# Kernel tuning notes

Measured on AMD Instinct MI355X. Metric: run time of the kernel, lower is better.

## Reference

```python
import jax, jax.numpy as jnp
import numpy as np

N_NODES = 100000
N_EDGES = 1600000
NFEAT, NHID, NCLASS = 512, 128, 40


def setup_inputs() -> dict:
    key = jax.random.key(0)
    ks = jax.random.split(key, 8)
    x = jax.random.normal(ks[0], (N_NODES, NFEAT), dtype=jnp.float32)
    adj_row = jax.random.randint(ks[1], (N_EDGES,), 0, N_NODES, dtype=jnp.int64)
    adj_col = jax.random.randint(ks[2], (N_EDGES,), 0, N_NODES, dtype=jnp.int64)
    adj_val = jax.random.uniform(ks[3], (N_EDGES,), dtype=jnp.float32)
    W1 = jax.random.normal(ks[4], (NFEAT, NHID), dtype=jnp.float32) * (1.0 / np.sqrt(NHID))
    b1 = jax.random.normal(ks[5], (NHID,), dtype=jnp.float32) * 0.01
    W2 = jax.random.normal(ks[6], (NHID, NCLASS), dtype=jnp.float32) * (1.0 / np.sqrt(NCLASS))
    b2 = jax.random.normal(ks[7], (NCLASS,), dtype=jnp.float32) * 0.01
    return {"x": x, "adj_row": adj_row, "adj_col": adj_col, "adj_val": adj_val,
            "W1": W1, "b1": b1, "W2": W2, "b2": b2}


def _spmm(row, col, val, dense):
    # COO SpMM: out[r] = sum_e val[e] * dense[col[e]]  for edges with row[e]==r
    gathered = val[:, None] * dense[col]          # [E, F]
    return jax.ops.segment_sum(gathered, row, num_segments=N_NODES)


def reference(x, adj_row, adj_col, adj_val, W1, b1, W2, b2):
    # Layer 1: support = X @ W1; out = A @ support + b1; ReLU
    h = _spmm(adj_row, adj_col, adj_val, x @ W1) + b1
    h = jax.nn.relu(h)
    # dropout is identity in eval mode (training=False)
    # Layer 2
    logits = _spmm(adj_row, adj_col, adj_val, h @ W2) + b2
    return jax.nn.log_softmax(logits, axis=1)
```

## Files before the change

kernel.cpp:

```cpp
#include <hip/hip_runtime.h>
#include <hip/hip_bf16.h>
#include <math.h>

#define N_NODES 100000
#define N_EDGES 1600000
#define NFEAT 512
#define NHID 128
#define NCLASS 40
#define CAP 48
#define G1_ROWS 128
#define G1_BLOCKS ((N_NODES + G1_ROWS - 1) / G1_ROWS)
#define PITCH 520

#define BIN_ROWS 256
#define NBINS ((N_NODES + BIN_ROWS - 1) / BIN_ROWS)
#define EPB 4096
#define P1_BLOCKS ((N_EDGES + EPB - 1) / EPB)

typedef __attribute__((ext_vector_type(8))) short short8;
typedef __attribute__((ext_vector_type(4))) float floatx4;

__device__ __forceinline__ short f2bf(float f) {
    union { float f; unsigned u; } v; v.f = f;
    unsigned r = v.u + 0x7FFFu + ((v.u >> 16) & 1u);
    return (short)(r >> 16);
}
__device__ __forceinline__ float bf2f(unsigned short u) {
    union { unsigned u; float f; } v; v.u = ((unsigned)u) << 16;
    return v.f;
}
__device__ __forceinline__ unsigned pk2bf(float a, float b) {
    __hip_bfloat162 t = __float22bfloat162_rn(make_float2(a, b));
    union { __hip_bfloat162 h; unsigned u; } v; v.h = t;
    return v.u;
}

__global__ void convert_W1_kernel(const float* __restrict__ W1, unsigned short* __restrict__ W1T) {
    int i = blockIdx.x * 256 + threadIdx.x;
    int k = i >> 7, n = i & 127;
    W1T[(size_t)n * NFEAT + k] = (unsigned short)f2bf(W1[i]);
}

__global__ __launch_bounds__(256)
void p1_hist_kernel(const int* __restrict__ adj_row, int* __restrict__ blockHistT) {
    __shared__ int hh[NBINS];
    int t = threadIdx.x;
    for (int i = t; i < NBINS; i += 256) hh[i] = 0;
    __syncthreads();
    int base = blockIdx.x * EPB;
    #pragma unroll
    for (int i = 0; i < EPB / 256; i++) {
        int e = base + i * 256 + t;
        if (e < N_EDGES) atomicAdd(&hh[adj_row[e] >> 8], 1);
    }
    __syncthreads();
    for (int i = t; i < NBINS; i += 256)
        blockHistT[(size_t)i * P1_BLOCKS + blockIdx.x] = hh[i];
}

__global__ __launch_bounds__(512)
void p1_rowscan_kernel(int* __restrict__ blockHistT, int* __restrict__ rowTotal) {
    __shared__ int s[512];
    int b = blockIdx.x, t = threadIdx.x;
    int v = (t < P1_BLOCKS) ? blockHistT[(size_t)b * P1_BLOCKS + t] : 0;
    s[t] = v;
    __syncthreads();
    for (int ofs = 1; ofs < 512; ofs <<= 1) {
        int w = (t >= ofs) ? s[t - ofs] : 0;
        __syncthreads();
        s[t] += w;
        __syncthreads();
    }
    if (t < P1_BLOCKS) blockHistT[(size_t)b * P1_BLOCKS + t] = s[t] - v;
    if (t == 511) rowTotal[b] = s[511];
}

__global__ __launch_bounds__(512)
void p1_binscan_kernel(const int* __restrict__ rowTotal, int* __restrict__ binBase) {
    __shared__ int s[512];
    int t = threadIdx.x;
    int v = (t < NBINS) ? rowTotal[t] : 0;
    s[t] = v;
    __syncthreads();
    for (int ofs = 1; ofs < 512; ofs <<= 1) {
        int w = (t >= ofs) ? s[t - ofs] : 0;
        __syncthreads();
        s[t] += w;
        __syncthreads();
    }
    if (t < NBINS) binBase[t] = s[t] - v;
    if (t == 511) binBase[NBINS] = s[511];
}

__global__ __launch_bounds__(256)
void p1_scatter_kernel(const int* __restrict__ adj_row, const int* __restrict__ adj_col,
                       const float* __restrict__ adj_val,
                       const int* __restrict__ blockHistT, const int* __restrict__ binBase,
                       int2* __restrict__ recs) {
    __shared__ int cur[NBINS];
    int t = threadIdx.x;
    for (int i = t; i < NBINS; i += 256)
        cur[i] = blockHistT[(size_t)i * P1_BLOCKS + blockIdx.x] + binBase[i];
    __syncthreads();
    int base = blockIdx.x * EPB;
    #pragma unroll
    for (int i = 0; i < EPB / 256; i++) {
        int e = base + i * 256 + t;
        if (e < N_EDGES) {
            int r = adj_row[e];
            int pos = atomicAdd(&cur[r >> 8], 1);
            recs[pos] = make_int2(((r & 255) << 17) | adj_col[e],
                                  __float_as_int(adj_val[e]));
        }
    }
}

__global__ __launch_bounds__(256)
void p2_fill_kernel(const int2* __restrict__ recs, const int* __restrict__ binBase,
                    int* __restrict__ counts, int2* __restrict__ csr) {
    __shared__ int cnt[BIN_ROWS];
    int b = blockIdx.x, t = threadIdx.x;
    cnt[t] = 0;
    __syncthreads();
    int beg = binBase[b];
    int end = binBase[b + 1];
    for (int i = beg + t; i < end; i += 256) {
        int2 rec = recs[i];
        int rl = ((unsigned)rec.x) >> 17;
        int col = rec.x & 0x1FFFF;
        int rank = atomicAdd(&cnt[rl], 1);
        if (rank < CAP)
            csr[(size_t)(b * BIN_ROWS + rl) * CAP + rank] = make_int2(col, rec.y);
    }
    __syncthreads();
    int row = b * BIN_ROWS + t;
    if (row < N_NODES) counts[row] = cnt[t];
}

__global__ __launch_bounds__(512)
void gemm1_kernel(const float* __restrict__ x, const unsigned short* __restrict__ W1T,
                  unsigned short* __restrict__ out) {
    __shared__ unsigned short Bs[NHID * PITCH];
    int t = threadIdx.x;
    {
        const short8* src = (const short8*)W1T;
        #pragma unroll
        for (int i = 0; i < 16; i++) {
            int c = t + i * 512;
            int row = c >> 6;
            int col = (c & 63) * 8;
            *(short8*)&Bs[row * PITCH + col] = src[c];
        }
    }
    __syncthreads();

    int w = t >> 6, l = t & 63;
    int lane16 = l & 15, quad = l >> 4;
    int rowBase = blockIdx.x * G1_ROWS + w * 16;

    floatx4 acc[8];
    #pragma unroll
    for (int j = 0; j < 8; j++) acc[j] = (floatx4){0.f, 0.f, 0.f, 0.f};

    int gr = rowBase + lane16;
    if (gr >= N_NODES) gr = N_NODES - 1;
    const float* aRow = x + (size_t)gr * NFEAT + quad * 8;

    #pragma unroll 4
    for (int kc = 0; kc < NFEAT; kc += 32) {
        float4 v0 = *(const float4*)(aRow + kc);
        float4 v1 = *(const float4*)(aRow + kc + 4);
        union { short8 s; unsigned u[4]; } av;
        av.u[0] = pk2bf(v0.x, v0.y);
        av.u[1] = pk2bf(v0.z, v0.w);
        av.u[2] = pk2bf(v1.x, v1.y);
        av.u[3] = pk2bf(v1.z, v1.w);
        short8 afr = av.s;
        #pragma unroll
        for (int nt = 0; nt < 8; nt++) {
            short8 bfr = *(const short8*)&Bs[(nt * 16 + lane16) * PITCH + kc + quad * 8];
            acc[nt] = __builtin_amdgcn_mfma_f32_16x16x32_bf16(afr, bfr, acc[nt], 0, 0, 0);
        }
    }
    #pragma unroll
    for (int r = 0; r < 4; r++) {
        int gr2 = rowBase + quad * 4 + r;
        if (gr2 < N_NODES) {
            #pragma unroll
            for (int nt = 0; nt < 8; nt++)
                out[(size_t)gr2 * NHID + nt * 16 + lane16] =
                    (unsigned short)f2bf(acc[nt][r]);
        }
    }
}

__global__ __launch_bounds__(256)
void spmmg_kernel(const int* __restrict__ counts, const int2* __restrict__ csr,
                  const unsigned short* __restrict__ dense, const float* __restrict__ b1,
                  const float* __restrict__ W2, unsigned short* __restrict__ out) {
    __shared__ float W2s[NHID * NCLASS];
    __shared__ float hs[32][NHID];
    int t = threadIdx.x;
    for (int i = t; i < NHID * NCLASS; i += 256) W2s[i] = W2[i];
    int w = t >> 6, l = t & 63;
    int row0 = blockIdx.x * 32;
    float b1l0 = b1[l * 2 + 0], b1l1 = b1[l * 2 + 1];

    for (int k = 0; k < 8; k++) {
        int r = row0 + w * 8 + k;
        int cnt = min(counts[r], CAP);
        int2 pk = (l < cnt) ? csr[(size_t)r * CAP + l] : make_int2(0, 0);
        float a0 = 0.f, a1 = 0.f;
        int j = 0;
        for (; j + 16 <= cnt; j += 16) {
            unsigned d[16];
            float v[16];
            #pragma unroll
            for (int q = 0; q < 16; q++) {
                int c = __shfl(pk.x, j + q);
                v[q] = __int_as_float(__shfl(pk.y, j + q));
                d[q] = *(const unsigned*)&dense[(size_t)c * NHID + l * 2];
            }
            #pragma unroll
            for (int q = 0; q < 16; q++) {
                a0 += v[q] * bf2f((unsigned short)d[q]);
                a1 += v[q] * bf2f((unsigned short)(d[q] >> 16));
            }
        }
        for (; j + 8 <= cnt; j += 8) {
            unsigned d[8];
            float v[8];
            #pragma unroll
            for (int q = 0; q < 8; q++) {
                int c = __shfl(pk.x, j + q);
                v[q] = __int_as_float(__shfl(pk.y, j + q));
                d[q] = *(const unsigned*)&dense[(size_t)c * NHID + l * 2];
            }
            #pragma unroll
            for (int q = 0; q < 8; q++) {
                a0 += v[q] * bf2f((unsigned short)d[q]);
                a1 += v[q] * bf2f((unsigned short)(d[q] >> 16));
            }
        }
        for (; j < cnt; j++) {
            int c = __shfl(pk.x, j);
            float v = __int_as_float(__shfl(pk.y, j));
            unsigned d = *(const unsigned*)&dense[(size_t)c * NHID + l * 2];
            a0 += v * bf2f((unsigned short)d);
            a1 += v * bf2f((unsigned short)(d >> 16));
        }
        *(float2*)&hs[w * 8 + k][l * 2] =
            make_float2(fmaxf(a0 + b1l0, 0.f), fmaxf(a1 + b1l1, 0.f));
    }
    __syncthreads();

    if (l < NCLASS) {
        float acc[8];
        #pragma unroll
        for (int j = 0; j < 8; j++) acc[j] = 0.f;
        #pragma unroll 4
        for (int k2 = 0; k2 < NHID; k2++) {
            float wk = W2s[k2 * NCLASS + l];
            #pragma unroll
            for (int j = 0; j < 8; j++) acc[j] += hs[w * 8 + j][k2] * wk;
        }
        #pragma unroll
        for (int j = 0; j < 8; j++)
            out[(size_t)(row0 + w * 8 + j) * NCLASS + l] = (unsigned short)f2bf(acc[j]);
    }
}

__global__ __launch_bounds__(256)
void spmm2_kernel(const int* __restrict__ counts, const int2* __restrict__ csr,
                  const unsigned short* __restrict__ dense, const float* __restrict__ b2,
                  float* __restrict__ out) {
    int r = blockIdx.x * 4 + (threadIdx.x >> 6);
    int l = threadIdx.x & 63;
    int cnt = min(counts[r], CAP);
    int2 pk = (l < cnt) ? csr[(size_t)r * CAP + l] : make_int2(0, 0);
    float acc = 0.f;
    int j = 0;
    for (; j + 16 <= cnt; j += 16) {
        float v[16], f[16];
        #pragma unroll
        for (int q = 0; q < 16; q++) {
            int c = __shfl(pk.x, j + q);
            v[q] = __int_as_float(__shfl(pk.y, j + q));
            f[q] = (l < NCLASS) ? bf2f(dense[(size_t)c * NCLASS + l]) : 0.f;
        }
        #pragma unroll
        for (int q = 0; q < 16; q++) acc += v[q] * f[q];
    }
    for (; j + 8 <= cnt; j += 8) {
        float v[8], f[8];
        #pragma unroll
        for (int q = 0; q < 8; q++) {
            int c = __shfl(pk.x, j + q);
            v[q] = __int_as_float(__shfl(pk.y, j + q));
            f[q] = (l < NCLASS) ? bf2f(dense[(size_t)c * NCLASS + l]) : 0.f;
        }
        #pragma unroll
        for (int q = 0; q < 8; q++) acc += v[q] * f[q];
    }
    for (; j < cnt; j++) {
        int c = __shfl(pk.x, j);
        float v = __int_as_float(__shfl(pk.y, j));
        if (l < NCLASS) acc += v * bf2f(dense[(size_t)c * NCLASS + l]);
    }
    float logit = (l < NCLASS) ? (acc + b2[l]) : -INFINITY;
    float m = logit;
    #pragma unroll
    for (int o = 32; o >= 1; o >>= 1) m = fmaxf(m, __shfl_xor(m, o, 64));
    float e = (l < NCLASS) ? __expf(logit - m) : 0.f;
    float s = e;
    #pragma unroll
    for (int o = 32; o >= 1; o >>= 1) s += __shfl_xor(s, o, 64);
    if (l < NCLASS) out[(size_t)r * NCLASS + l] = logit - m - __logf(s);
}


extern "C" void kernel_launch(void* const* d_in, const int* in_sizes, int n_in,
                              void* d_out, int out_size, void* d_ws, size_t ws_size,
                              hipStream_t stream) {
    const float* x       = (const float*)d_in[0];
    const int*   adj_row = (const int*)d_in[1];
    const int*   adj_col = (const int*)d_in[2];
    const float* adj_val = (const float*)d_in[3];
    const float* W1      = (const float*)d_in[4];
    const float* b1      = (const float*)d_in[5];
    const float* W2      = (const float*)d_in[6];
    const float* b2      = (const float*)d_in[7];
    float* out = (float*)d_out;

    char* ws = (char*)d_ws;
    size_t off = 0;
    auto alloc = [&](size_t bytes) -> void* {
        void* p = ws + off;
        off += bytes;
        off = (off + 255) & ~(size_t)255;
        return p;
    };
    unsigned short* support1 = (unsigned short*)alloc((size_t)N_NODES * NHID * 2);
    unsigned short* support2 = (unsigned short*)alloc((size_t)N_NODES * NCLASS * 2);
    unsigned short* W1T      = (unsigned short*)alloc((size_t)NFEAT * NHID * 2);
    int*   counts     = (int*)alloc((size_t)N_NODES * 4);
    int2*  csr        = (int2*)alloc((size_t)N_NODES * CAP * 8);
    int*   blockHistT = (int*)alloc((size_t)NBINS * P1_BLOCKS * 4);
    int*   rowTotal   = (int*)alloc((size_t)NBINS * 4);
    int*   binBase    = (int*)alloc((size_t)(NBINS + 1) * 4);
    int2*  recs       = (int2*)support1;

    convert_W1_kernel<<<(NFEAT * NHID) / 256, 256, 0, stream>>>(W1, W1T);
    p1_hist_kernel<<<P1_BLOCKS, 256, 0, stream>>>(adj_row, blockHistT);
    p1_rowscan_kernel<<<NBINS, 512, 0, stream>>>(blockHistT, rowTotal);
    p1_binscan_kernel<<<1, 512, 0, stream>>>(rowTotal, binBase);
    p1_scatter_kernel<<<P1_BLOCKS, 256, 0, stream>>>(adj_row, adj_col, adj_val,
                                                     blockHistT, binBase, recs);
    p2_fill_kernel<<<NBINS, 256, 0, stream>>>(recs, binBase, counts, csr);
    gemm1_kernel<<<G1_BLOCKS, 512, 0, stream>>>(x, W1T, support1);
    spmmg_kernel<<<N_NODES / 32, 256, 0, stream>>>(counts, csr, support1, b1, W2, support2);
    spmm2_kernel<<<N_NODES / 4, 256, 0, stream>>>(counts, csr, support2, b2, out);
}
```

Before: 610.0 us.

## Split GEMM1 K staging, scalarize CSR edge loads, and keep hidden activations in bf16

GEMM1 now stages W1 into shared memory in two K halves with a smaller pitch. This roughly halves LDS use per block, so more blocks can be resident per CU, at the cost of an extra barrier and a second staging pass. Both SpMM kernels make the row index wave-uniform via readfirstlane and read CSR entries directly, which the compiler can turn into scalar loads instead of per-edge cross-lane shuffles. The fused SpMM+GEMM2 kernel stores the ReLU output in shared memory as packed bf16, adds less shared-memory traffic, and drops the block barrier after the hidden-row loop, relying on each wave reading only its own rows.

Result: faster. 591.7 us (-3.0%).

```diff
diff --git a/kernel.cpp b/kernel.cpp
--- a/kernel.cpp
+++ b/kernel.cpp
@@ -10,7 +10,8 @@
 #define CAP 48
 #define G1_ROWS 128
 #define G1_BLOCKS ((N_NODES + G1_ROWS - 1) / G1_ROWS)
-#define PITCH 520
+#define HKW 256
+#define PITCH2 264
 
 #define BIN_ROWS 256
 #define NBINS ((N_NODES + BIN_ROWS - 1) / BIN_ROWS)
@@ -140,20 +141,8 @@
 __global__ __launch_bounds__(512)
 void gemm1_kernel(const float* __restrict__ x, const unsigned short* __restrict__ W1T,
                   unsigned short* __restrict__ out) {
-    __shared__ unsigned short Bs[NHID * PITCH];
-    int t = threadIdx.x;
-    {
-        const short8* src = (const short8*)W1T;
-        #pragma unroll
-        for (int i = 0; i < 16; i++) {
-            int c = t + i * 512;
-            int row = c >> 6;
-            int col = (c & 63) * 8;
-            *(short8*)&Bs[row * PITCH + col] = src[c];
-        }
-    }
-    __syncthreads();
-
+    __shared__ unsigned short Bs[NHID * PITCH2];
+    int t = threadIdx.x;
     int w = t >> 6, l = t & 63;
     int lane16 = l & 15, quad = l >> 4;
     int rowBase = blockIdx.x * G1_ROWS + w * 16;
@@ -164,22 +153,36 @@
 
     int gr = rowBase + lane16;
     if (gr >= N_NODES) gr = N_NODES - 1;
-    const float* aRow = x + (size_t)gr * NFEAT + quad * 8;
-
-    #pragma unroll 4
-    for (int kc = 0; kc < NFEAT; kc += 32) {
-        float4 v0 = *(const float4*)(aRow + kc);
-        float4 v1 = *(const float4*)(aRow + kc + 4);
-        union { short8 s; unsigned u[4]; } av;
-        av.u[0] = pk2bf(v0.x, v0.y);
-        av.u[1] = pk2bf(v0.z, v0.w);
-        av.u[2] = pk2bf(v1.x, v1.y);
-        av.u[3] = pk2bf(v1.z, v1.w);
-        short8 afr = av.s;
-        #pragma unroll
-        for (int nt = 0; nt < 8; nt++) {
-            short8 bfr = *(const short8*)&Bs[(nt * 16 + lane16) * PITCH + kc + quad * 8];
-            acc[nt] = __builtin_amdgcn_mfma_f32_16x16x32_bf16(afr, bfr, acc[nt], 0, 0, 0);
+
+    for (int kh = 0; kh < 2; kh++) {
+        if (kh) __syncthreads();
+        {
+            const unsigned short* src = W1T + kh * HKW;
+            #pragma unroll
+            for (int i = 0; i < 8; i++) {
+                int c = t + i * 512;
+                int n = c >> 5;
+                int off = (c & 31) * 8;
+                *(short8*)&Bs[n * PITCH2 + off] = *(const short8*)&src[(size_t)n * NFEAT + off];
+            }
+        }
+        __syncthreads();
+        const float* aRowH = x + (size_t)gr * NFEAT + kh * HKW + quad * 8;
+        #pragma unroll 4
+        for (int kc = 0; kc < HKW; kc += 32) {
+            float4 v0 = *(const float4*)(aRowH + kc);
+            float4 v1 = *(const float4*)(aRowH + kc + 4);
+            union { short8 s; unsigned u[4]; } av;
+            av.u[0] = pk2bf(v0.x, v0.y);
+            av.u[1] = pk2bf(v0.z, v0.w);
+            av.u[2] = pk2bf(v1.x, v1.y);
+            av.u[3] = pk2bf(v1.z, v1.w);
+            short8 afr = av.s;
+            #pragma unroll
+            for (int nt = 0; nt < 8; nt++) {
+                short8 bfr = *(const short8*)&Bs[(nt * 16 + lane16) * PITCH2 + kc + quad * 8];
+                acc[nt] = __builtin_amdgcn_mfma_f32_16x16x32_bf16(afr, bfr, acc[nt], 0, 0, 0);
+            }
         }
     }
     #pragma unroll
@@ -199,17 +202,18 @@
                   const unsigned short* __restrict__ dense, const float* __restrict__ b1,
                   const float* __restrict__ W2, unsigned short* __restrict__ out) {
     __shared__ float W2s[NHID * NCLASS];
-    __shared__ float hs[32][NHID];
+    __shared__ unsigned hs32[32][64];
     int t = threadIdx.x;
     for (int i = t; i < NHID * NCLASS; i += 256) W2s[i] = W2[i];
+    __syncthreads();
     int w = t >> 6, l = t & 63;
     int row0 = blockIdx.x * 32;
     float b1l0 = b1[l * 2 + 0], b1l1 = b1[l * 2 + 1];
 
     for (int k = 0; k < 8; k++) {
-        int r = row0 + w * 8 + k;
-        int cnt = min(counts[r], CAP);
-        int2 pk = (l < cnt) ? csr[(size_t)r * CAP + l] : make_int2(0, 0);
+        int rs = __builtin_amdgcn_readfirstlane(row0 + w * 8 + k);
+        int cnt = min(counts[rs], CAP);
+        const int2* rowCsr = csr + (size_t)rs * CAP;
         float a0 = 0.f, a1 = 0.f;
         int j = 0;
         for (; j + 16 <= cnt; j += 16) {
@@ -217,9 +221,9 @@
             float v[16];
             #pragma unroll
             for (int q = 0; q < 16; q++) {
-                int c = __shfl(pk.x, j + q);
-                v[q] = __int_as_float(__shfl(pk.y, j + q));
-                d[q] = *(const unsigned*)&dense[(size_t)c * NHID + l * 2];
+                int2 e = rowCsr[j + q];
+                v[q] = __int_as_float(e.y);
+                d[q] = *(const unsigned*)&dense[(size_t)e.x * NHID + l * 2];
             }
             #pragma unroll
             for (int q = 0; q < 16; q++) {
@@ -232,9 +236,9 @@
             float v[8];
             #pragma unroll
             for (int q = 0; q < 8; q++) {
-                int c = __shfl(pk.x, j + q);
-                v[q] = __int_as_float(__shfl(pk.y, j + q));
-                d[q] = *(const unsigned*)&dense[(size_t)c * NHID + l * 2];
+                int2 e = rowCsr[j + q];
+                v[q] = __int_as_float(e.y);
+                d[q] = *(const unsigned*)&dense[(size_t)e.x * NHID + l * 2];
             }
             #pragma unroll
             for (int q = 0; q < 8; q++) {
@@ -243,26 +247,28 @@
             }
         }
         for (; j < cnt; j++) {
-            int c = __shfl(pk.x, j);
-            float v = __int_as_float(__shfl(pk.y, j));
-            unsigned d = *(const unsigned*)&dense[(size_t)c * NHID + l * 2];
+            int2 e = rowCsr[j];
+            float v = __int_as_float(e.y);
+            unsigned d = *(const unsigned*)&dense[(size_t)e.x * NHID + l * 2];
             a0 += v * bf2f((unsigned short)d);
             a1 += v * bf2f((unsigned short)(d >> 16));
         }
-        *(float2*)&hs[w * 8 + k][l * 2] =
-            make_float2(fmaxf(a0 + b1l0, 0.f), fmaxf(a1 + b1l1, 0.f));
-    }
-    __syncthreads();
-
+        hs32[w * 8 + k][l] = pk2bf(fmaxf(a0 + b1l0, 0.f), fmaxf(a1 + b1l1, 0.f));
+    }
     if (l < NCLASS) {
         float acc[8];
         #pragma unroll
         for (int j = 0; j < 8; j++) acc[j] = 0.f;
         #pragma unroll 4
-        for (int k2 = 0; k2 < NHID; k2++) {
-            float wk = W2s[k2 * NCLASS + l];
-            #pragma unroll
-            for (int j = 0; j < 8; j++) acc[j] += hs[w * 8 + j][k2] * wk;
+        for (int k2 = 0; k2 < NHID; k2 += 2) {
+            float wk0 = W2s[k2 * NCLASS + l];
+            float wk1 = W2s[(k2 + 1) * NCLASS + l];
+            #pragma unroll
+            for (int j = 0; j < 8; j++) {
+                unsigned u = hs32[w * 8 + j][k2 >> 1];
+                acc[j] += bf2f((unsigned short)u) * wk0
+                        + bf2f((unsigned short)(u >> 16)) * wk1;
+            }
         }
         #pragma unroll
         for (int j = 0; j < 8; j++)
@@ -274,19 +280,19 @@
 void spmm2_kernel(const int* __restrict__ counts, const int2* __restrict__ csr,
                   const unsigned short* __restrict__ dense, const float* __restrict__ b2,
                   float* __restrict__ out) {
-    int r = blockIdx.x * 4 + (threadIdx.x >> 6);
+    int rs = __builtin_amdgcn_readfirstlane(blockIdx.x * 4 + (threadIdx.x >> 6));
     int l = threadIdx.x & 63;
-    int cnt = min(counts[r], CAP);
-    int2 pk = (l < cnt) ? csr[(size_t)r * CAP + l] : make_int2(0, 0);
+    int cnt = min(counts[rs], CAP);
+    const int2* rowCsr = csr + (size_t)rs * CAP;
     float acc = 0.f;
     int j = 0;
     for (; j + 16 <= cnt; j += 16) {
         float v[16], f[16];
         #pragma unroll
         for (int q = 0; q < 16; q++) {
-            int c = __shfl(pk.x, j + q);
-            v[q] = __int_as_float(__shfl(pk.y, j + q));
-            f[q] = (l < NCLASS) ? bf2f(dense[(size_t)c * NCLASS + l]) : 0.f;
+            int2 e = rowCsr[j + q];
+            v[q] = __int_as_float(e.y);
+            f[q] = (l < NCLASS) ? bf2f(dense[(size_t)e.x * NCLASS + l]) : 0.f;
         }
         #pragma unroll
         for (int q = 0; q < 16; q++) acc += v[q] * f[q];
@@ -295,17 +301,17 @@
         float v[8], f[8];
         #pragma unroll
         for (int q = 0; q < 8; q++) {
-            int c = __shfl(pk.x, j + q);
-            v[q] = __int_as_float(__shfl(pk.y, j + q));
-            f[q] = (l < NCLASS) ? bf2f(dense[(size_t)c * NCLASS + l]) : 0.f;
+            int2 e = rowCsr[j + q];
+            v[q] = __int_as_float(e.y);
+            f[q] = (l < NCLASS) ? bf2f(dense[(size_t)e.x * NCLASS + l]) : 0.f;
         }
         #pragma unroll
         for (int q = 0; q < 8; q++) acc += v[q] * f[q];
     }
     for (; j < cnt; j++) {
-        int c = __shfl(pk.x, j);
-        float v = __int_as_float(__shfl(pk.y, j));
-        if (l < NCLASS) acc += v * bf2f(dense[(size_t)c * NCLASS + l]);
+        int2 e = rowCsr[j];
+        float v = __int_as_float(e.y);
+        if (l < NCLASS) acc += v * bf2f(dense[(size_t)e.x * NCLASS + l]);
     }
     float logit = (l < NCLASS) ? (acc + b2[l]) : -INFINITY;
     float m = logit;
@@ -315,7 +321,7 @@
     float s = e;
     #pragma unroll
     for (int o = 32; o >= 1; o >>= 1) s += __shfl_xor(s, o, 64);
-    if (l < NCLASS) out[(size_t)r * NCLASS + l] = logit - m - __logf(s);
+    if (l < NCLASS) out[(size_t)rs * NCLASS + l] = logit - m - __logf(s);
 }
 
 
```
